# Kernel tuning notes

Hardware: AMD Instinct MI355X
Metric: run time of the kernel (lower is better)

The kernel has to match this reference:

```python
import jax, jax.numpy as jnp
import numpy as np

B, N, C = 32, 256, 4096
H = 16
HEAD_DIM = C // H  # 256 == N, required by the module's math
SCALE = HEAD_DIM ** -0.5


def setup_inputs() -> dict:
    key = jax.random.key(0)
    ks = jax.random.split(key, 7)
    std = C ** -0.5
    return {
        "x1": jax.random.normal(ks[0], (B, N, C), dtype=jnp.float32),
        "x2": jax.random.normal(ks[1], (B, N, C), dtype=jnp.float32),
        "Wq": jax.random.normal(ks[2], (C, C), dtype=jnp.float32) * std,
        "Wk": jax.random.normal(ks[3], (C, C), dtype=jnp.float32) * std,
        "Wv": jax.random.normal(ks[4], (C, C), dtype=jnp.float32) * std,
        "Wp": jax.random.normal(ks[5], (C, C), dtype=jnp.float32) * std,
        "bp": jnp.zeros((C,), dtype=jnp.float32),
    }


def reference(x1, x2, Wq, Wk, Wv, Wp, bp):
    b, n, c = x1.shape
    h, hd = H, HEAD_DIM
    # QKV projections (qkv_bias=False); q pre-scaled as in source
    q = (x1 @ Wq.T) * SCALE
    k = x2 @ Wk.T
    v = x2 @ Wv.T
    split = lambda t: t.reshape(b, n, h, hd).transpose(0, 2, 1, 3)  # b h n hd
    q, k, v = split(q), split(k), split(v)
    # channel-wise attention: q^T @ k over the token axis -> [b, h, hd, hd]
    attn = jax.nn.softmax(jnp.einsum("bhni,bhnj->bhij", q, k), axis=-1)
    # attn @ v: inner dim of attn (hd) contracts with token axis of v (n == hd)
    out = jnp.einsum("bhin,bhnc->bhic", attn, v)  # [b, h, hd, hd]
    out = out.transpose(0, 2, 1, 3).reshape(b, n, c)
    x = out @ Wp.T + bp
    return (x, attn)
```

## Files before the change

kernel.cpp:

```cpp
#include <hip/hip_runtime.h>

typedef __attribute__((ext_vector_type(4))) float f32x4;
typedef __attribute__((ext_vector_type(8))) short short8;
typedef __attribute__((ext_vector_type(4))) unsigned short ushort4v;

__device__ __forceinline__ unsigned short rne_bf16(float f) {
  unsigned int u = __builtin_bit_cast(unsigned int, f);
  u += 0x7FFFu + ((u >> 16) & 1u);
  return (unsigned short)(u >> 16);
}

__device__ __forceinline__ void async16(void* lds, const void* g) {
  __builtin_amdgcn_global_load_lds(
      (const __attribute__((address_space(1))) void*)g,
      (__attribute__((address_space(3))) void*)lds, 16, 0, 0);
}

__device__ __forceinline__ f32x4 mfma16(short8 a, short8 b, f32x4 c) {
  return __builtin_amdgcn_mfma_f32_16x16x32_bf16(a, b, c, 0, 0, 0);
}

__global__ __launch_bounds__(256) void cast_k(const float* __restrict__ in,
                                              unsigned short* __restrict__ out,
                                              int n4) {
  int stride = gridDim.x * 256;
  for (int i = blockIdx.x * 256 + threadIdx.x; i < n4; i += stride) {
    float4 v = ((const float4*)in)[i];
    ushort4v o = {rne_bf16(v.x), rne_bf16(v.y), rne_bf16(v.z), rne_bf16(v.w)};
    ((ushort4v*)out)[i] = o;
  }
}

template <int MODE>
__global__ __launch_bounds__(512, 2) void gemm256(const unsigned short* __restrict__ A,
                                                  const unsigned short* __restrict__ B,
                                                  float* __restrict__ outF,
                                                  unsigned short* __restrict__ outB,
                                                  const float* __restrict__ bias,
                                                  int K, int lda, int ldb,
                                                  float scale, int gx) {
  __shared__ unsigned short lds[65536];
  const int tid = threadIdx.x;
  const int lane = tid & 63;
  const int wid = tid >> 6;
  const int wm = wid >> 2;
  const int wn = wid & 3;
  int lin = blockIdx.x;
  lin = (lin & 7) * (gridDim.x >> 3) + (lin >> 3);
  const int bx = lin % gx;
  const int by = lin / gx;
  const int m0 = by * 256, n0 = bx * 256;
  const int NT = K >> 6;

  const int gsw8 = (((tid & 3) ^ ((tid >> 3) & 3))) * 8;
  const unsigned short* gA = A + (size_t)(m0 + (tid >> 2)) * lda + gsw8;
  const unsigned short* gB = B + (size_t)(n0 + (tid >> 2)) * ldb + gsw8;
  const size_t astep = (size_t)128 * lda;
  const size_t bstep = (size_t)128 * ldb;
  unsigned short* ld0 = &lds[tid * 8];

#define STG_A(Q) do { \
    const int kt_ = ((Q) >> 1) * 64 + ((Q) & 1) * 32; \
    const int off_ = (((Q) >> 1) & 1) * 32768 + ((Q) & 1) * 8192; \
    const unsigned short* sA_ = gA + kt_; \
    unsigned short* dA_ = ld0 + off_; \
    async16(dA_, sA_); async16(dA_ + 4096, sA_ + astep); } while (0)
#define STG_B(Q) do { \
    const int kt_ = ((Q) >> 1) * 64 + ((Q) & 1) * 32; \
    const int off_ = 16384 + (((Q) >> 1) & 1) * 32768 + ((Q) & 1) * 8192; \
    const unsigned short* sB_ = gB + kt_; \
    unsigned short* dB_ = ld0 + off_; \
    async16(dB_, sB_); async16(dB_ + 4096, sB_ + bstep); } while (0)

  const int rl = lane & 15;
  const int ch = (lane >> 4) ^ ((rl >> 1) & 3);
  const int aidx = wm * 4096 + rl * 32 + ch * 8;
  const int bidx = 16384 + wn * 2048 + rl * 32 + ch * 8;

  short8 af[8], bf[4];
#define READ_A4(base, o) do { \
    _Pragma("unroll") \
    for (int r_ = 0; r_ < 4; ++r_) \
      af[(o) + r_] = *(const short8*)&lds[(base) + aidx + ((o) + r_) * 512]; \
  } while (0)
#define READ_B4(base) do { \
    _Pragma("unroll") \
    for (int s_ = 0; s_ < 4; ++s_) bf[s_] = *(const short8*)&lds[(base) + bidx + s_ * 512]; \
  } while (0)

  f32x4 acc[8][4];
#pragma unroll
  for (int r = 0; r < 8; ++r)
#pragma unroll
    for (int s = 0; s < 4; ++s) acc[r][s] = (f32x4){0.f, 0.f, 0.f, 0.f};

#define MFMA16(o) do { \
    _Pragma("unroll") \
    for (int r_ = 0; r_ < 4; ++r_) \
      _Pragma("unroll") \
      for (int s_ = 0; s_ < 4; ++s_) \
        acc[(o) + r_][s_] = mfma16(af[(o) + r_], bf[s_], acc[(o) + r_][s_]); \
  } while (0)

#define PHASE(P_, rb_, doStage_) do { \
    READ_A4((rb_), 0); \
    READ_B4((rb_)); \
    if (doStage_) STG_A((P_) + 3); \
    __builtin_amdgcn_sched_barrier(0); \
    __builtin_amdgcn_s_barrier(); \
    asm volatile("s_waitcnt lgkmcnt(0)" ::: "memory"); \
    __builtin_amdgcn_sched_barrier(0); \
    __builtin_amdgcn_s_setprio(1); \
    MFMA16(0); \
    __builtin_amdgcn_s_setprio(0); \
    __builtin_amdgcn_s_barrier(); \
    READ_A4((rb_), 4); \
    if (doStage_) STG_B((P_) + 3); \
    __builtin_amdgcn_sched_barrier(0); \
    __builtin_amdgcn_s_barrier(); \
    asm volatile("s_waitcnt lgkmcnt(0)" ::: "memory"); \
    __builtin_amdgcn_sched_barrier(0); \
    __builtin_amdgcn_s_setprio(1); \
    MFMA16(4); \
    __builtin_amdgcn_s_setprio(0); \
    if (doStage_) asm volatile("s_waitcnt vmcnt(4)" ::: "memory"); \
    else          asm volatile("s_waitcnt vmcnt(0)" ::: "memory"); \
    __builtin_amdgcn_s_barrier(); \
  } while (0)

  STG_A(0); STG_B(0); STG_A(1); STG_B(1); STG_A(2); STG_B(2);
  asm volatile("s_waitcnt vmcnt(4)" ::: "memory");
  __builtin_amdgcn_s_barrier();

  const int PMAX = 2 * NT - 1;
  for (int t = 0; t < NT; ++t) {
    const int bb = (t & 1) * 32768;
    PHASE(2 * t,     bb,        (2 * t + 3) <= PMAX);
    PHASE(2 * t + 1, bb + 8192, (2 * t + 4) <= PMAX);
  }
#undef STG_A
#undef STG_B
#undef READ_A4
#undef READ_B4
#undef MFMA16
#undef PHASE

  const int fcol = lane & 15;
  const int frow = (lane >> 4) * 4;
#pragma unroll
  for (int r = 0; r < 8; ++r) {
#pragma unroll
    for (int s = 0; s < 4; ++s) {
      f32x4 v = acc[r][s];
      const int m = m0 + wm * 128 + r * 16 + frow;
      const int n = n0 + wn * 64 + s * 16 + fcol;
      if (MODE == 0) {
        ushort4v p;
#pragma unroll
        for (int j = 0; j < 4; ++j) p[j] = rne_bf16(v[j] * scale);
        size_t d = ((size_t)((m >> 8) * 16 + (n >> 8))) * 65536 +
                   (size_t)(n & 255) * 256 + (m & 255);
        *(ushort4v*)&outB[d] = p;
      } else {
        float bv = bias[n];
#pragma unroll
        for (int j = 0; j < 4; ++j) outF[(size_t)(m + j) * 4096 + n] = v[j] + bv;
      }
    }
  }
}

template <int MODE>
__global__ __launch_bounds__(256) void gemm_bt(const unsigned short* __restrict__ Ab,
                                               const unsigned short* __restrict__ Bb,
                                               float* __restrict__ outF,
                                               unsigned short* __restrict__ outB,
                                               int K, int lda, int ldb) {
  __shared__ short Ash[128 * 32];
  __shared__ short Bsh[128 * 32];

  const int tid = threadIdx.x;
  const int lane = tid & 63;
  const int wid = tid >> 6;
  const int z = blockIdx.z;
  const int m0 = blockIdx.y * 128;
  const int n0 = blockIdx.x * 128;

  const unsigned short* A = Ab + (size_t)z * 65536;
  const unsigned short* B = Bb + (size_t)z * 65536;

  const int wm = (wid >> 1) * 64;
  const int wn = (wid & 1) * 64;
  const int fcol = lane & 15;
  const int kslot = (lane >> 4) * 8;

  f32x4 acc[4][4];
#pragma unroll
  for (int r = 0; r < 4; ++r)
#pragma unroll
    for (int s = 0; s < 4; ++s) acc[r][s] = (f32x4){0.f, 0.f, 0.f, 0.f};

  const int arow = tid >> 2;
  const int acol = (tid & 3) * 8;
  const unsigned short* gA = A + (size_t)(m0 + arow) * lda + acol;
  const unsigned short* gB = B + (size_t)(n0 + arow) * ldb + acol;
  short* lA = &Ash[tid * 8];
  short* lB = &Bsh[tid * 8];

  for (int kt = 0; kt < K; kt += 32) {
    __syncthreads();
    async16(lA, gA + kt);
    async16(lA + 2048, gA + (size_t)64 * lda + kt);
    async16(lB, gB + kt);
    async16(lB + 2048, gB + (size_t)64 * ldb + kt);
    __syncthreads();

    short8 a[4], b[4];
#pragma unroll
    for (int r = 0; r < 4; ++r)
      a[r] = *(const short8*)&Ash[(wm + r * 16 + fcol) * 32 + kslot];
#pragma unroll
    for (int s = 0; s < 4; ++s)
      b[s] = *(const short8*)&Bsh[(wn + s * 16 + fcol) * 32 + kslot];
#pragma unroll
    for (int r = 0; r < 4; ++r)
#pragma unroll
      for (int s = 0; s < 4; ++s)
        acc[r][s] = __builtin_amdgcn_mfma_f32_16x16x32_bf16(a[r], b[s], acc[r][s], 0, 0, 0);
  }

  const int frow = (lane >> 4) * 4;
#pragma unroll
  for (int r = 0; r < 4; ++r) {
#pragma unroll
    for (int s = 0; s < 4; ++s) {
      f32x4 v = acc[r][s];
      const int m = m0 + wm + r * 16 + frow;
      const int n = n0 + wn + s * 16 + fcol;
      if (MODE == 1) {
        float* C = outF + (size_t)z * 65536;
#pragma unroll
        for (int j = 0; j < 4; ++j) C[(size_t)(m + j) * 256 + n] = v[j];
      } else {
        size_t base = ((size_t)((z >> 4) * 256 + m)) * 4096 + (z & 15) * 256 + n;
#pragma unroll
        for (int j = 0; j < 4; ++j) outB[base + (size_t)j * 4096] = rne_bf16(v[j]);
      }
    }
  }
}

__global__ __launch_bounds__(256) void softmax_k(float* __restrict__ S,
                                                 unsigned short* __restrict__ P) {
  const int lane = threadIdx.x & 63;
  const size_t row = (size_t)blockIdx.x * 4 + (threadIdx.x >> 6);
  float4 x = *(const float4*)&S[row * 256 + lane * 4];
  float mx = fmaxf(fmaxf(x.x, x.y), fmaxf(x.z, x.w));
#pragma unroll
  for (int off = 32; off; off >>= 1) mx = fmaxf(mx, __shfl_xor(mx, off, 64));
  float e0 = __expf(x.x - mx), e1 = __expf(x.y - mx);
  float e2 = __expf(x.z - mx), e3 = __expf(x.w - mx);
  float s = e0 + e1 + e2 + e3;
#pragma unroll
  for (int off = 32; off; off >>= 1) s += __shfl_xor(s, off, 64);
  const float inv = 1.0f / s;
  e0 *= inv; e1 *= inv; e2 *= inv; e3 *= inv;
  *(float4*)&S[row * 256 + lane * 4] = make_float4(e0, e1, e2, e3);
  ushort4v ob = {rne_bf16(e0), rne_bf16(e1), rne_bf16(e2), rne_bf16(e3)};
  *(ushort4v*)&P[row * 256 + lane * 4] = ob;
}

extern "C" void kernel_launch(void* const* d_in, const int* in_sizes, int n_in,
                              void* d_out, int out_size, void* d_ws, size_t ws_size,
                              hipStream_t stream) {
  const float* x1 = (const float*)d_in[0];
  const float* x2 = (const float*)d_in[1];
  const float* Wq = (const float*)d_in[2];
  const float* Wk = (const float*)d_in[3];
  const float* Wv = (const float*)d_in[4];
  const float* Wp = (const float*)d_in[5];
  const float* bp = (const float*)d_in[6];

  float* outX = (float*)d_out;
  float* outA = outX + (size_t)33554432;

  unsigned short* Qt  = (unsigned short*)d_ws;
  unsigned short* Kt  = Qt + 33554432;
  unsigned short* Vt  = Kt + 33554432;
  unsigned short* x1b = Vt + 33554432;
  unsigned short* x2b = x1b + 33554432;
  unsigned short* Wb  = x2b + 33554432;

  const float SCALE = 0.0625f;

  cast_k<<<2048, 256, 0, stream>>>(x1, x1b, 8388608);
  cast_k<<<2048, 256, 0, stream>>>(x2, x2b, 8388608);

  cast_k<<<2048, 256, 0, stream>>>(Wq, Wb, 4194304);
  gemm256<0><<<512, 512, 0, stream>>>(x1b, Wb, nullptr, Qt, nullptr,
                                      4096, 4096, 4096, SCALE, 16);
  cast_k<<<2048, 256, 0, stream>>>(Wk, Wb, 4194304);
  gemm256<0><<<512, 512, 0, stream>>>(x2b, Wb, nullptr, Kt, nullptr,
                                      4096, 4096, 4096, 1.0f, 16);
  cast_k<<<2048, 256, 0, stream>>>(Wv, Wb, 4194304);
  gemm256<0><<<512, 512, 0, stream>>>(x2b, Wb, nullptr, Vt, nullptr,
                                      4096, 4096, 4096, 1.0f, 16);

  gemm_bt<1><<<dim3(2, 2, 512), 256, 0, stream>>>(Qt, Kt, outA, nullptr, 256, 256, 256);
  softmax_k<<<32768, 256, 0, stream>>>(outA, x1b);
  gemm_bt<2><<<dim3(2, 2, 512), 256, 0, stream>>>(x1b, Vt, nullptr, x2b, 256, 256, 256);

  cast_k<<<2048, 256, 0, stream>>>(Wp, Wb, 4194304);
  gemm256<3><<<512, 512, 0, stream>>>(x2b, Wb, outX, nullptr, bp,
                                      4096, 4096, 4096, 1.0f, 16);
}
```

Before: 1.349 ms.

## Switch big GEMMs to 32x32 MFMA, simplify pipeline, fuse QK^T with softmax

The main projection GEMM moves from 16x16x32 to 32x32x16 bf16 MFMA, which changes fragment layout, LDS read indexing and the epilogue. Its phase schedule drops from two barrier-separated halves to one read/stage/compute block per phase. Separately, the q·k GEMM and the softmax are merged into one kernel that reduces row max and sum across waves through LDS, so the fp32 attention matrix is no longer written and then read back by a second pass. Removing the intra-phase barriers and lgkmcnt waits may reduce overlap or cause LDS hazards. The fused kernel also writes its fp32 and bf16 outputs with scattered scalar stores.

```diff
diff --git a/kernel.cpp b/kernel.cpp
--- a/kernel.cpp
+++ b/kernel.cpp
@@ -1,6 +1,7 @@
 #include <hip/hip_runtime.h>
 
 typedef __attribute__((ext_vector_type(4))) float f32x4;
+typedef __attribute__((ext_vector_type(16))) float f32x16;
 typedef __attribute__((ext_vector_type(8))) short short8;
 typedef __attribute__((ext_vector_type(4))) unsigned short ushort4v;
 
@@ -18,6 +19,9 @@
 
 __device__ __forceinline__ f32x4 mfma16(short8 a, short8 b, f32x4 c) {
   return __builtin_amdgcn_mfma_f32_16x16x32_bf16(a, b, c, 0, 0, 0);
+}
+__device__ __forceinline__ f32x16 mfma32(short8 a, short8 b, f32x16 c) {
+  return __builtin_amdgcn_mfma_f32_32x32x16_bf16(a, b, c, 0, 0, 0);
 }
 
 __global__ __launch_bounds__(256) void cast_k(const float* __restrict__ in,
@@ -72,60 +76,48 @@
     unsigned short* dB_ = ld0 + off_; \
     async16(dB_, sB_); async16(dB_ + 4096, sB_ + bstep); } while (0)
 
-  const int rl = lane & 15;
-  const int ch = (lane >> 4) ^ ((rl >> 1) & 3);
-  const int aidx = wm * 4096 + rl * 32 + ch * 8;
-  const int bidx = 16384 + wn * 2048 + rl * 32 + ch * 8;
+  const int l31 = lane & 31;
+  const int hi = lane >> 5;
+  const int q4 = (l31 >> 1) & 3;
+  const int co0 = ((hi) ^ q4) * 8;
+  const int co1 = ((2 + hi) ^ q4) * 8;
+  const int abase = (wm * 128 + l31) * 32;
+  const int bbase = 16384 + (wn * 64 + l31) * 32;
 
   short8 af[8], bf[4];
-#define READ_A4(base, o) do { \
+#define READ12(base) do { \
     _Pragma("unroll") \
-    for (int r_ = 0; r_ < 4; ++r_) \
-      af[(o) + r_] = *(const short8*)&lds[(base) + aidx + ((o) + r_) * 512]; \
+    for (int f_ = 0; f_ < 4; ++f_) { \
+      af[f_]     = *(const short8*)&lds[(base) + abase + f_ * 1024 + co0]; \
+      af[4 + f_] = *(const short8*)&lds[(base) + abase + f_ * 1024 + co1]; \
+    } \
+    bf[0] = *(const short8*)&lds[(base) + bbase + co0]; \
+    bf[1] = *(const short8*)&lds[(base) + bbase + 1024 + co0]; \
+    bf[2] = *(const short8*)&lds[(base) + bbase + co1]; \
+    bf[3] = *(const short8*)&lds[(base) + bbase + 1024 + co1]; \
   } while (0)
-#define READ_B4(base) do { \
+
+  f32x16 acc[4][2];
+#pragma unroll
+  for (int f = 0; f < 4; ++f)
+#pragma unroll
+    for (int g = 0; g < 2; ++g)
+#pragma unroll
+      for (int e = 0; e < 16; ++e) acc[f][g][e] = 0.f;
+
+#define MFMA16() do { \
+    __builtin_amdgcn_s_setprio(1); \
     _Pragma("unroll") \
-    for (int s_ = 0; s_ < 4; ++s_) bf[s_] = *(const short8*)&lds[(base) + bidx + s_ * 512]; \
-  } while (0)
-
-  f32x4 acc[8][4];
-#pragma unroll
-  for (int r = 0; r < 8; ++r)
-#pragma unroll
-    for (int s = 0; s < 4; ++s) acc[r][s] = (f32x4){0.f, 0.f, 0.f, 0.f};
-
-#define MFMA16(o) do { \
+    for (int f_ = 0; f_ < 4; ++f_) \
+      _Pragma("unroll") \
+      for (int g_ = 0; g_ < 2; ++g_) \
+        acc[f_][g_] = mfma32(af[f_], bf[g_], acc[f_][g_]); \
     _Pragma("unroll") \
-    for (int r_ = 0; r_ < 4; ++r_) \
+    for (int f_ = 0; f_ < 4; ++f_) \
       _Pragma("unroll") \
-      for (int s_ = 0; s_ < 4; ++s_) \
-        acc[(o) + r_][s_] = mfma16(af[(o) + r_], bf[s_], acc[(o) + r_][s_]); \
-  } while (0)
-
-#define PHASE(P_, rb_, doStage_) do { \
-    READ_A4((rb_), 0); \
-    READ_B4((rb_)); \
-    if (doStage_) STG_A((P_) + 3); \
-    __builtin_amdgcn_sched_barrier(0); \
-    __builtin_amdgcn_s_barrier(); \
-    asm volatile("s_waitcnt lgkmcnt(0)" ::: "memory"); \
-    __builtin_amdgcn_sched_barrier(0); \
-    __builtin_amdgcn_s_setprio(1); \
-    MFMA16(0); \
+      for (int g_ = 0; g_ < 2; ++g_) \
+        acc[f_][g_] = mfma32(af[4 + f_], bf[2 + g_], acc[f_][g_]); \
     __builtin_amdgcn_s_setprio(0); \
-    __builtin_amdgcn_s_barrier(); \
-    READ_A4((rb_), 4); \
-    if (doStage_) STG_B((P_) + 3); \
-    __builtin_amdgcn_sched_barrier(0); \
-    __builtin_amdgcn_s_barrier(); \
-    asm volatile("s_waitcnt lgkmcnt(0)" ::: "memory"); \
-    __builtin_amdgcn_sched_barrier(0); \
-    __builtin_amdgcn_s_setprio(1); \
-    MFMA16(4); \
-    __builtin_amdgcn_s_setprio(0); \
-    if (doStage_) asm volatile("s_waitcnt vmcnt(4)" ::: "memory"); \
-    else          asm volatile("s_waitcnt vmcnt(0)" ::: "memory"); \
-    __builtin_amdgcn_s_barrier(); \
   } while (0)
 
   STG_A(0); STG_B(0); STG_A(1); STG_B(1); STG_A(2); STG_B(2);
@@ -135,36 +127,168 @@
   const int PMAX = 2 * NT - 1;
   for (int t = 0; t < NT; ++t) {
     const int bb = (t & 1) * 32768;
-    PHASE(2 * t,     bb,        (2 * t + 3) <= PMAX);
-    PHASE(2 * t + 1, bb + 8192, (2 * t + 4) <= PMAX);
+    {
+      READ12(bb);
+      const bool st = (2 * t + 3) <= PMAX;
+      if (st) { STG_A(2 * t + 3); STG_B(2 * t + 3); }
+      MFMA16();
+      if (st) asm volatile("s_waitcnt vmcnt(4)" ::: "memory");
+      else    asm volatile("s_waitcnt vmcnt(0)" ::: "memory");
+      __builtin_amdgcn_s_barrier();
+    }
+    {
+      READ12(bb + 8192);
+      const bool st = (2 * t + 4) <= PMAX;
+      if (st) { STG_A(2 * t + 4); STG_B(2 * t + 4); }
+      MFMA16();
+      if (st) asm volatile("s_waitcnt vmcnt(4)" ::: "memory");
+      else    asm volatile("s_waitcnt vmcnt(0)" ::: "memory");
+      __builtin_amdgcn_s_barrier();
+    }
   }
 #undef STG_A
 #undef STG_B
-#undef READ_A4
-#undef READ_B4
+#undef READ12
 #undef MFMA16
-#undef PHASE
-
+
+#pragma unroll
+  for (int f = 0; f < 4; ++f) {
+#pragma unroll
+    for (int g = 0; g < 2; ++g) {
+      f32x16 v = acc[f][g];
+      const int mb = m0 + wm * 128 + f * 32;
+      const int n = n0 + wn * 64 + g * 32 + l31;
+      if (MODE == 0) {
+        const size_t hb = ((size_t)((m0 >> 8) * 16 + (n >> 8))) * 65536 +
+                          (size_t)(n & 255) * 256;
+#pragma unroll
+        for (int qq = 0; qq < 4; ++qq) {
+          ushort4v p;
+#pragma unroll
+          for (int j = 0; j < 4; ++j) p[j] = rne_bf16(v[qq * 4 + j] * scale);
+          const int tok = (mb & 255) + qq * 8 + hi * 4;
+          *(ushort4v*)&outB[hb + tok] = p;
+        }
+      } else {
+        const float bv = bias[n];
+#pragma unroll
+        for (int qq = 0; qq < 4; ++qq)
+#pragma unroll
+          for (int j = 0; j < 4; ++j) {
+            const int m = mb + qq * 8 + hi * 4 + j;
+            outF[(size_t)m * 4096 + n] = v[qq * 4 + j] + bv;
+          }
+      }
+    }
+  }
+}
+
+__global__ __launch_bounds__(256) void sgemm_sm(const unsigned short* __restrict__ Qt,
+                                                const unsigned short* __restrict__ Kt,
+                                                float* __restrict__ outA,
+                                                unsigned short* __restrict__ Pb) {
+  __shared__ short Ash[128 * 32];
+  __shared__ short Bsh[256 * 32];
+  __shared__ float redM[128][2];
+  __shared__ float redS[128][2];
+
+  const int tid = threadIdx.x;
+  const int lane = tid & 63;
+  const int wid = tid >> 6;
+  const int z = blockIdx.y;
+  const int m0 = blockIdx.x * 128;
+  const int wm = wid >> 1;
+  const int wn = wid & 1;
   const int fcol = lane & 15;
+  const int kslot = (lane >> 4) * 8;
   const int frow = (lane >> 4) * 4;
-#pragma unroll
-  for (int r = 0; r < 8; ++r) {
-#pragma unroll
-    for (int s = 0; s < 4; ++s) {
-      f32x4 v = acc[r][s];
-      const int m = m0 + wm * 128 + r * 16 + frow;
-      const int n = n0 + wn * 64 + s * 16 + fcol;
-      if (MODE == 0) {
-        ushort4v p;
-#pragma unroll
-        for (int j = 0; j < 4; ++j) p[j] = rne_bf16(v[j] * scale);
-        size_t d = ((size_t)((m >> 8) * 16 + (n >> 8))) * 65536 +
-                   (size_t)(n & 255) * 256 + (m & 255);
-        *(ushort4v*)&outB[d] = p;
-      } else {
-        float bv = bias[n];
-#pragma unroll
-        for (int j = 0; j < 4; ++j) outF[(size_t)(m + j) * 4096 + n] = v[j] + bv;
+
+  const unsigned short* Ah = Qt + (size_t)z * 65536;
+  const unsigned short* Bh = Kt + (size_t)z * 65536;
+
+  f32x4 acc[4][8];
+#pragma unroll
+  for (int r = 0; r < 4; ++r)
+#pragma unroll
+    for (int s = 0; s < 8; ++s) acc[r][s] = (f32x4){0.f, 0.f, 0.f, 0.f};
+
+  const int arow = tid >> 2;
+  const int acol = (tid & 3) * 8;
+  const unsigned short* gA = Ah + (size_t)(m0 + arow) * 256 + acol;
+  const unsigned short* gB = Bh + (size_t)arow * 256 + acol;
+  short* lA = &Ash[tid * 8];
+  short* lB = &Bsh[tid * 8];
+
+  for (int kt = 0; kt < 256; kt += 32) {
+    __syncthreads();
+    async16(lA, gA + kt);
+    async16(lA + 2048, gA + (size_t)64 * 256 + kt);
+    async16(lB, gB + kt);
+    async16(lB + 2048, gB + (size_t)64 * 256 + kt);
+    async16(lB + 4096, gB + (size_t)128 * 256 + kt);
+    async16(lB + 6144, gB + (size_t)192 * 256 + kt);
+    __syncthreads();
+
+    short8 a[4], b[8];
+#pragma unroll
+    for (int r = 0; r < 4; ++r)
+      a[r] = *(const short8*)&Ash[(wm * 64 + r * 16 + fcol) * 32 + kslot];
+#pragma unroll
+    for (int s = 0; s < 8; ++s)
+      b[s] = *(const short8*)&Bsh[(wn * 128 + s * 16 + fcol) * 32 + kslot];
+#pragma unroll
+    for (int r = 0; r < 4; ++r)
+#pragma unroll
+      for (int s = 0; s < 8; ++s)
+        acc[r][s] = mfma16(a[r], b[s], acc[r][s]);
+  }
+  __syncthreads();
+
+#pragma unroll
+  for (int r = 0; r < 4; ++r) {
+#pragma unroll
+    for (int j = 0; j < 4; ++j) {
+      float m = acc[r][0][j];
+#pragma unroll
+      for (int s = 1; s < 8; ++s) m = fmaxf(m, acc[r][s][j]);
+#pragma unroll
+      for (int off = 1; off < 16; off <<= 1) m = fmaxf(m, __shfl_xor(m, off, 64));
+      if (fcol == 0) redM[wm * 64 + r * 16 + frow + j][wn] = m;
+    }
+  }
+  __syncthreads();
+#pragma unroll
+  for (int r = 0; r < 4; ++r) {
+#pragma unroll
+    for (int j = 0; j < 4; ++j) {
+      const int rl = wm * 64 + r * 16 + frow + j;
+      const float m = fmaxf(redM[rl][0], redM[rl][1]);
+      float sum = 0.f;
+#pragma unroll
+      for (int s = 0; s < 8; ++s) {
+        float e = __expf(acc[r][s][j] - m);
+        acc[r][s][j] = e;
+        sum += e;
+      }
+#pragma unroll
+      for (int off = 1; off < 16; off <<= 1) sum += __shfl_xor(sum, off, 64);
+      if (fcol == 0) redS[rl][wn] = sum;
+    }
+  }
+  __syncthreads();
+#pragma unroll
+  for (int r = 0; r < 4; ++r) {
+#pragma unroll
+    for (int j = 0; j < 4; ++j) {
+      const int rl = wm * 64 + r * 16 + frow + j;
+      const float inv = 1.0f / (redS[rl][0] + redS[rl][1]);
+      const size_t rowo = (size_t)z * 65536 + (size_t)(m0 + rl) * 256;
+#pragma unroll
+      for (int s = 0; s < 8; ++s) {
+        const float p = acc[r][s][j] * inv;
+        const size_t o = rowo + wn * 128 + s * 16 + fcol;
+        outA[o] = p;
+        Pb[o] = rne_bf16(p);
       }
     }
   }
@@ -226,7 +350,7 @@
     for (int r = 0; r < 4; ++r)
 #pragma unroll
       for (int s = 0; s < 4; ++s)
-        acc[r][s] = __builtin_amdgcn_mfma_f32_16x16x32_bf16(a[r], b[s], acc[r][s], 0, 0, 0);
+        acc[r][s] = mfma16(a[r], b[s], acc[r][s]);
   }
 
   const int frow = (lane >> 4) * 4;
@@ -237,37 +361,11 @@
       f32x4 v = acc[r][s];
       const int m = m0 + wm + r * 16 + frow;
       const int n = n0 + wn + s * 16 + fcol;
-      if (MODE == 1) {
-        float* C = outF + (size_t)z * 65536;
-#pragma unroll
-        for (int j = 0; j < 4; ++j) C[(size_t)(m + j) * 256 + n] = v[j];
-      } else {
-        size_t base = ((size_t)((z >> 4) * 256 + m)) * 4096 + (z & 15) * 256 + n;
-#pragma unroll
-        for (int j = 0; j < 4; ++j) outB[base + (size_t)j * 4096] = rne_bf16(v[j]);
-      }
-    }
-  }
-}
-
-__global__ __launch_bounds__(256) void softmax_k(float* __restrict__ S,
-                                                 unsigned short* __restrict__ P) {
-  const int lane = threadIdx.x & 63;
-  const size_t row = (size_t)blockIdx.x * 4 + (threadIdx.x >> 6);
-  float4 x = *(const float4*)&S[row * 256 + lane * 4];
-  float mx = fmaxf(fmaxf(x.x, x.y), fmaxf(x.z, x.w));
-#pragma unroll
-  for (int off = 32; off; off >>= 1) mx = fmaxf(mx, __shfl_xor(mx, off, 64));
-  float e0 = __expf(x.x - mx), e1 = __expf(x.y - mx);
-  float e2 = __expf(x.z - mx), e3 = __expf(x.w - mx);
-  float s = e0 + e1 + e2 + e3;
-#pragma unroll
-  for (int off = 32; off; off >>= 1) s += __shfl_xor(s, off, 64);
-  const float inv = 1.0f / s;
-  e0 *= inv; e1 *= inv; e2 *= inv; e3 *= inv;
-  *(float4*)&S[row * 256 + lane * 4] = make_float4(e0, e1, e2, e3);
-  ushort4v ob = {rne_bf16(e0), rne_bf16(e1), rne_bf16(e2), rne_bf16(e3)};
-  *(ushort4v*)&P[row * 256 + lane * 4] = ob;
+      size_t base = ((size_t)((z >> 4) * 256 + m)) * 4096 + (z & 15) * 256 + n;
+#pragma unroll
+      for (int j = 0; j < 4; ++j) outB[base + (size_t)j * 4096] = rne_bf16(v[j]);
+    }
+  }
 }
 
 extern "C" void kernel_launch(void* const* d_in, const int* in_sizes, int n_in,
@@ -306,8 +404,7 @@
   gemm256<0><<<512, 512, 0, stream>>>(x2b, Wb, nullptr, Vt, nullptr,
                                       4096, 4096, 4096, 1.0f, 16);
 
-  gemm_bt<1><<<dim3(2, 2, 512), 256, 0, stream>>>(Qt, Kt, outA, nullptr, 256, 256, 256);
-  softmax_k<<<32768, 256, 0, stream>>>(outA, x1b);
+  sgemm_sm<<<dim3(2, 512), 256, 0, stream>>>(Qt, Kt, outA, x1b);
   gemm_bt<2><<<dim3(2, 2, 512), 256, 0, stream>>>(x1b, Vt, nullptr, x2b, 256, 256, 256);
 
   cast_k<<<2048, 256, 0, stream>>>(Wp, Wb, 4194304);
```

Measured after the change: 1.417 ms. +5.1%, slower.
